# Optimization experiments

Hardware: AMD Instinct MI355X
Metric: run time of the kernel (lower is better)

## Reference

```python
import jax, jax.numpy as jnp
import numpy as np

N_NODES = 50000
N_EDGES = 800000
F_IN = 512
H1 = 64
H2 = 128
N_CLASSES = 10
N_GRAPHS = 64


def _sage_conv(x, src, dst, w_l, b_l, w_r, n_nodes):
    # mean-aggregate neighbor features (messages flow src -> dst), then
    # out = lin_l(mean_neigh) + lin_r(x)   (PyG SAGEConv defaults)
    msg = x[src]                                           # [E, F] gather
    agg = jax.ops.segment_sum(msg, dst, num_segments=n_nodes)
    deg = jax.ops.segment_sum(jnp.ones((src.shape[0], 1), x.dtype), dst,
                              num_segments=n_nodes)
    mean = agg / jnp.maximum(deg, 1.0)                     # 0 for isolated nodes
    return mean @ w_l + b_l + x @ w_r


def setup_inputs() -> dict:
    key = jax.random.key(0)
    ks = jax.random.split(key, 12)
    x = jax.random.normal(ks[0], (N_NODES, F_IN), dtype=jnp.float32)
    edge_index = jax.random.randint(ks[1], (2, N_EDGES), 0, N_NODES, dtype=jnp.int64)
    batch = jnp.sort(jax.random.randint(ks[2], (N_NODES,), 0, N_GRAPHS, dtype=jnp.int64))

    def glorot(k, fan_in, fan_out):
        s = jnp.sqrt(6.0 / (fan_in + fan_out)).astype(jnp.float32)
        return jax.random.uniform(k, (fan_in, fan_out), jnp.float32, -s, s)

    return {
        "x": x, "edge_index": edge_index, "batch": batch,
        "w1_l": glorot(ks[3], F_IN, H1), "b1_l": jnp.zeros((H1,), jnp.float32),
        "w1_r": glorot(ks[4], F_IN, H1),
        "w2_l": glorot(ks[5], H1, H2), "b2_l": jnp.zeros((H2,), jnp.float32),
        "w2_r": glorot(ks[6], H1, H2),
        "w_fc": glorot(ks[7], H2, N_CLASSES),
        "b_fc": jnp.zeros((N_CLASSES,), jnp.float32),
    }


def reference(x, edge_index, batch, w1_l, b1_l, w1_r, w2_l, b2_l, w2_r, w_fc, b_fc):
    src, dst = edge_index[0], edge_index[1]
    n = x.shape[0]
    h = jax.nn.relu(_sage_conv(x, src, dst, w1_l, b1_l, w1_r, n))
    # dropout is identity in eval mode
    h = _sage_conv(h, src, dst, w2_l, b2_l, w2_r, n)        # [N, H2]
    # global mean pool over graphs
    summed = jax.ops.segment_sum(h, batch, num_segments=N_GRAPHS)
    cnt = jax.ops.segment_sum(jnp.ones((n, 1), h.dtype), batch, num_segments=N_GRAPHS)
    pooled = summed / jnp.maximum(cnt, 1.0)                 # [G, H2]
    logits = pooled @ w_fc + b_fc                           # [G, C]
    return jax.nn.log_softmax(logits, axis=1)
```

## Files before the change

### kernel.cpp

```cpp
#include <hip/hip_runtime.h>

#define NN 50000
#define NE 800000
#define FIN 512
#define H1DIM 64
#define H2DIM 128
#define NC 10
#define NG 64
#define NRT 3125
#define SB 196
#define SORT_THREADS (SB * 256)

typedef __attribute__((ext_vector_type(8))) short bf16x8;
typedef __attribute__((ext_vector_type(4))) float f32x4;

__device__ inline short f2bf(float f) {
  unsigned u = __float_as_uint(f);
  unsigned r = u + 0x7fffu + ((u >> 16) & 1u);
  return (short)(r >> 16);
}
__device__ inline float bf2f(short s) {
  return __uint_as_float(((unsigned)(unsigned short)s) << 16);
}

__device__ __forceinline__ void gbar(int* bar, int id) {
  __syncthreads();
  if (threadIdx.x == 0) {
    __threadfence();
    atomicAdd(&bar[id], 1);
    while (atomicAdd(&bar[id], 0) < SB) {}
  }
  __syncthreads();
}

__global__ __launch_bounds__(256) void sort_kernel(
    const int* __restrict__ src, const int* __restrict__ dst,
    int* __restrict__ cnt, int* __restrict__ rowptr, int* __restrict__ cursor,
    int* __restrict__ bsum, int* __restrict__ ssrc, int* __restrict__ bar) {
  const int b = blockIdx.x;
  const int t = threadIdx.x;
  const int idx = b * 256 + t;
  __shared__ int s[256];

  {
    int i = ((b + 98) % SB) * 256 + t;
    if (i < NN) cnt[i] = 0;
  }
  gbar(bar, 0);

  for (int j = idx; j < NE / 4; j += SORT_THREADS) {
    int4 d = *(const int4*)(dst + j * 4);
    atomicAdd(&cnt[d.x], 1);
    atomicAdd(&cnt[d.y], 1);
    atomicAdd(&cnt[d.z], 1);
    atomicAdd(&cnt[d.w], 1);
  }
  gbar(bar, 1);

  int v = (idx < NN) ? atomicAdd(&cnt[idx], 0) : 0;
  s[t] = v;
  __syncthreads();
  for (int off = 1; off < 256; off <<= 1) {
    int u = (t >= off) ? s[t - off] : 0;
    __syncthreads();
    s[t] += u;
    __syncthreads();
  }
  if (idx < NN) rowptr[idx] = s[t] - v;
  if (t == 255) bsum[b] = s[255];
  gbar(bar, 2);

  int bv = (t < SB) ? atomicAdd(&bsum[t], 0) : 0;
  s[t] = bv;
  __syncthreads();
  for (int off = 1; off < 256; off <<= 1) {
    int u = (t >= off) ? s[t - off] : 0;
    __syncthreads();
    s[t] += u;
    __syncthreads();
  }
  int prefix = (b == 0) ? 0 : s[b - 1];
  if (idx < NN) {
    int p = rowptr[idx] + prefix;
    rowptr[idx] = p;
    cursor[idx] = p;
  }
  if (idx == 0) rowptr[NN] = NE;
  gbar(bar, 3);

  for (int j = idx; j < NE / 4; j += SORT_THREADS) {
    int4 sv = *(const int4*)(src + j * 4);
    int4 dv = *(const int4*)(dst + j * 4);
    int p0 = atomicAdd(&cursor[dv.x], 1); ssrc[p0] = sv.x;
    int p1 = atomicAdd(&cursor[dv.y], 1); ssrc[p1] = sv.y;
    int p2 = atomicAdd(&cursor[dv.z], 1); ssrc[p2] = sv.z;
    int p3 = atomicAdd(&cursor[dv.w], 1); ssrc[p3] = sv.w;
  }
}

__global__ __launch_bounds__(256) void wbtf_prep_kernel(
    const float* __restrict__ wl, const float* __restrict__ wr,
    short* __restrict__ wbtf) {
  int w = blockIdx.x * 4 + (threadIdx.x >> 6);
  int lane = threadIdx.x & 63;
  int ni = w >> 4;
  int ks = w & 15;
  int n = ni * 16 + (lane & 15);
  int k = ks * 32 + (lane >> 4) * 8;
  bf16x8 o;
#pragma unroll
  for (int j = 0; j < 8; j++) {
    float v = (n < 64) ? wl[(size_t)(k + j) * 64 + n]
                       : wr[(size_t)(k + j) * 64 + (n - 64)];
    o[j] = f2bf(v);
  }
  *(bf16x8*)(wbtf + ((size_t)w * 64 + lane) * 8) = o;
}

__global__ __launch_bounds__(256) void gemm1_kernel(
    const float* __restrict__ x, const short* __restrict__ wbtf,
    short* __restrict__ xwl, float* __restrict__ xwr) {
  int w = blockIdx.x * 4 + (threadIdx.x >> 6);
  if (w >= NRT) return;
  int lane = threadIdx.x & 63;
  int l15 = lane & 15;
  int q = lane >> 4;
  const float* px = x + (size_t)(w * 16 + l15) * FIN + q * 8;
  const short* pb = wbtf + (size_t)lane * 8;

  const f32x4 z = {0.f, 0.f, 0.f, 0.f};
  f32x4 acc[8];
#pragma unroll
  for (int ni = 0; ni < 8; ni++) acc[ni] = z;

  float4 av0, av1, nv0, nv1;
  bf16x8 B0[8], B1[8];
  av0 = *(const float4*)(px);
  av1 = *(const float4*)(px + 4);
#pragma unroll
  for (int ni = 0; ni < 8; ni++)
    B0[ni] = *(const bf16x8*)(pb + (size_t)ni * 8192);

#pragma unroll
  for (int ks = 0; ks < 16; ks += 2) {
    if (ks + 1 < 16) {
      nv0 = *(const float4*)(px + (ks + 1) * 32);
      nv1 = *(const float4*)(px + (ks + 1) * 32 + 4);
#pragma unroll
      for (int ni = 0; ni < 8; ni++)
        B1[ni] = *(const bf16x8*)(pb + (size_t)ni * 8192 + (ks + 1) * 512);
    }
    {
      bf16x8 af;
      af[0] = f2bf(av0.x); af[1] = f2bf(av0.y);
      af[2] = f2bf(av0.z); af[3] = f2bf(av0.w);
      af[4] = f2bf(av1.x); af[5] = f2bf(av1.y);
      af[6] = f2bf(av1.z); af[7] = f2bf(av1.w);
#pragma unroll
      for (int ni = 0; ni < 8; ni++)
        acc[ni] = __builtin_amdgcn_mfma_f32_16x16x32_bf16(af, B0[ni], acc[ni], 0, 0, 0);
    }
    if (ks + 2 < 16) {
      av0 = *(const float4*)(px + (ks + 2) * 32);
      av1 = *(const float4*)(px + (ks + 2) * 32 + 4);
#pragma unroll
      for (int ni = 0; ni < 8; ni++)
        B0[ni] = *(const bf16x8*)(pb + (size_t)ni * 8192 + (ks + 2) * 512);
    }
    {
      bf16x8 af;
      af[0] = f2bf(nv0.x); af[1] = f2bf(nv0.y);
      af[2] = f2bf(nv0.z); af[3] = f2bf(nv0.w);
      af[4] = f2bf(nv1.x); af[5] = f2bf(nv1.y);
      af[6] = f2bf(nv1.z); af[7] = f2bf(nv1.w);
#pragma unroll
      for (int ni = 0; ni < 8; ni++)
        acc[ni] = __builtin_amdgcn_mfma_f32_16x16x32_bf16(af, B1[ni], acc[ni], 0, 0, 0);
    }
  }

  int row_base = w * 16 + q * 4;
#pragma unroll
  for (int ni = 0; ni < 8; ni++) {
    int col = ni * 16 + l15;
    int c = col & 63;
#pragma unroll
    for (int r = 0; r < 4; r++) {
      int row = row_base + r;
      if (col < 64) xwl[(size_t)row * 64 + c] = f2bf(acc[ni][r]);
      else          xwr[(size_t)row * 64 + c] = acc[ni][r];
    }
  }
}

__global__ __launch_bounds__(256) void agg1_h1_kernel(
    const int* __restrict__ rowptr, const int* __restrict__ ssrc,
    const short* __restrict__ xwl, const float* __restrict__ xwr,
    const float* __restrict__ b1, short* __restrict__ h1) {
  int node = blockIdx.x * 4 + (threadIdx.x >> 6);
  if (node >= NN) return;
  int lane = threadIdx.x & 63;
  int c = lane & 7;
  int r = lane >> 3;
  int lo = rowptr[node], hi = rowptr[node + 1];
  float acc[8];
#pragma unroll
  for (int k = 0; k < 8; k++) acc[k] = 0.f;
  for (int e = lo + r; e < hi; e += 8) {
    int s = ssrc[e];
    bf16x8 v = *(const bf16x8*)(xwl + (size_t)s * 64 + c * 8);
#pragma unroll
    for (int k = 0; k < 8; k++) acc[k] += bf2f(v[k]);
  }
#pragma unroll
  for (int k = 0; k < 8; k++) {
    acc[k] += __shfl_xor(acc[k], 8);
    acc[k] += __shfl_xor(acc[k], 16);
    acc[k] += __shfl_xor(acc[k], 32);
  }
  if (r == 0) {
    float dg = fmaxf((float)(hi - lo), 1.0f);
    const float* xr = xwr + (size_t)node * 64 + c * 8;
    bf16x8 out;
#pragma unroll
    for (int k = 0; k < 8; k++) {
      float v = fmaxf(acc[k] / dg + b1[c * 8 + k] + xr[k], 0.f);
      out[k] = f2bf(v);
    }
    *(bf16x8*)(h1 + (size_t)node * 64 + c * 8) = out;
  }
}

__global__ __launch_bounds__(256) void agg2_kernel(
    const int* __restrict__ rowptr, const int* __restrict__ ssrc,
    const short* __restrict__ h1, float* __restrict__ agg2) {
  int node = blockIdx.x * 4 + (threadIdx.x >> 6);
  if (node >= NN) return;
  int lane = threadIdx.x & 63;
  int c = lane & 7;
  int r = lane >> 3;
  int lo = rowptr[node], hi = rowptr[node + 1];
  float acc[8];
#pragma unroll
  for (int k = 0; k < 8; k++) acc[k] = 0.f;
  for (int e = lo + r; e < hi; e += 8) {
    int s = ssrc[e];
    bf16x8 v = *(const bf16x8*)(h1 + (size_t)s * 64 + c * 8);
#pragma unroll
    for (int k = 0; k < 8; k++) acc[k] += bf2f(v[k]);
  }
#pragma unroll
  for (int k = 0; k < 8; k++) {
    acc[k] += __shfl_xor(acc[k], 8);
    acc[k] += __shfl_xor(acc[k], 16);
    acc[k] += __shfl_xor(acc[k], 32);
  }
  if (r == 0) {
    float* p = agg2 + (size_t)node * 64 + c * 8;
    f32x4 lo4 = {acc[0], acc[1], acc[2], acc[3]};
    f32x4 hi4 = {acc[4], acc[5], acc[6], acc[7]};
    *(f32x4*)(p) = lo4;
    *(f32x4*)(p + 4) = hi4;
  }
}

__global__ __launch_bounds__(256) void pool1_kernel(
    const int* __restrict__ batch, const float* __restrict__ agg2,
    const short* __restrict__ h1, const int* __restrict__ rowptr,
    float* __restrict__ poolA, float* __restrict__ poolB,
    float* __restrict__ poolCnt) {
  int t = threadIdx.x;
  int c = t & 15;
  int s = t >> 4;
  int n0 = blockIdx.x * 256 + s * 16;
  int n1 = n0 + 16;
  if (n1 > NN) n1 = NN;

  f32x4 aA = {0.f, 0.f, 0.f, 0.f};
  f32x4 aB = {0.f, 0.f, 0.f, 0.f};
  int cur_g = -1;
  float run = 0.f;
  for (int n = n0; n < n1; n++) {
    int g = batch[n];
    if (g != cur_g) {
      if (cur_g >= 0) {
        float* pa = poolA + (size_t)cur_g * 64 + c * 4;
        float* pb = poolB + (size_t)cur_g * 64 + c * 4;
#pragma unroll
        for (int k = 0; k < 4; k++) {
          atomicAdd(&pa[k], aA[k]);
          atomicAdd(&pb[k], aB[k]);
        }
        if (c == 0) atomicAdd(&poolCnt[cur_g], run);
      }
      cur_g = g;
      aA = (f32x4){0.f, 0.f, 0.f, 0.f};
      aB = (f32x4){0.f, 0.f, 0.f, 0.f};
      run = 0.f;
    }
    float rd = 1.0f / fmaxf((float)(rowptr[n + 1] - rowptr[n]), 1.0f);
    f32x4 a2 = *(const f32x4*)(agg2 + (size_t)n * 64 + c * 4);
    const short* hp = h1 + (size_t)n * 64 + c * 4;
#pragma unroll
    for (int k = 0; k < 4; k++) {
      aA[k] = fmaf(a2[k], rd, aA[k]);
      aB[k] += bf2f(hp[k]);
    }
    run += 1.f;
  }
  if (cur_g >= 0) {
    float* pa = poolA + (size_t)cur_g * 64 + c * 4;
    float* pb = poolB + (size_t)cur_g * 64 + c * 4;
#pragma unroll
    for (int k = 0; k < 4; k++) {
      atomicAdd(&pa[k], aA[k]);
      atomicAdd(&pb[k], aB[k]);
    }
    if (c == 0) atomicAdd(&poolCnt[cur_g], run);
  }
}

__global__ __launch_bounds__(128) void final_kernel(
    const float* __restrict__ poolA, const float* __restrict__ poolB,
    const float* __restrict__ poolCnt, const float* __restrict__ w2l,
    const float* __restrict__ w2r, const float* __restrict__ b2,
    const float* __restrict__ wfc, const float* __restrict__ bfc,
    float* __restrict__ out) {
  int g = blockIdx.x;
  int j = threadIdx.x;
  __shared__ float sp[H2DIM];
  __shared__ float sl[NC];

  float invc = 1.0f / fmaxf(poolCnt[g], 1.0f);
  float v = b2[j];
  for (int k = 0; k < 64; k++) {
    float a = poolA[g * 64 + k] * invc;
    float b = poolB[g * 64 + k] * invc;
    v = fmaf(a, w2l[k * 128 + j], v);
    v = fmaf(b, w2r[k * 128 + j], v);
  }
  sp[j] = v;
  __syncthreads();
  if (j < NC) {
    float lg = bfc[j];
    for (int k = 0; k < H2DIM; k++) lg = fmaf(sp[k], wfc[k * NC + j], lg);
    sl[j] = lg;
  }
  __syncthreads();
  if (j < NC) {
    float m = -1e30f;
    for (int k = 0; k < NC; k++) m = fmaxf(m, sl[k]);
    float s = 0.f;
    for (int k = 0; k < NC; k++) s += expf(sl[k] - m);
    out[g * NC + j] = sl[j] - m - logf(s);
  }
}

extern "C" void kernel_launch(void* const* d_in, const int* in_sizes, int n_in,
                              void* d_out, int out_size, void* d_ws,
                              size_t ws_size, hipStream_t stream) {
  const float* x   = (const float*)d_in[0];
  const int* edge  = (const int*)d_in[1];
  const int* batch = (const int*)d_in[2];
  const float* w1l = (const float*)d_in[3];
  const float* b1l = (const float*)d_in[4];
  const float* w1r = (const float*)d_in[5];
  const float* w2l = (const float*)d_in[6];
  const float* b2l = (const float*)d_in[7];
  const float* w2r = (const float*)d_in[8];
  const float* wfc = (const float*)d_in[9];
  const float* bfc = (const float*)d_in[10];
  float* out = (float*)d_out;

  const int* src = edge;
  const int* dst = edge + NE;

  const size_t NF = (size_t)NN * 64;
  int*   bar     = (int*)d_ws;
  float* poolA   = (float*)(bar + 8);
  float* poolB   = poolA + (size_t)NG * 64;
  float* poolCnt = poolB + (size_t)NG * 64;
  int*   cnt     = (int*)(poolCnt + NG);
  int*   cursor  = cnt + NN;
  int*   rowptr  = cursor + NN;
  int*   bsum    = rowptr + 50004;
  int*   ssrc    = bsum + 256;
  short* xwl     = (short*)(ssrc + NE);
  short* h1s     = xwl + NF;
  short* wbtf    = h1s + NF;
  float* xwr     = (float*)(wbtf + 65536);
  float* agg2    = xwr + NF;

  hipMemsetAsync(bar, 0, (8 + 2 * NG * 64 + NG) * sizeof(int), stream);

  wbtf_prep_kernel<<<32, 256, 0, stream>>>(w1l, w1r, wbtf);
  sort_kernel<<<SB, 256, 0, stream>>>(src, dst, cnt, rowptr, cursor, bsum, ssrc, bar);
  gemm1_kernel<<<(NRT + 3) / 4, 256, 0, stream>>>(x, wbtf, xwl, xwr);

  agg1_h1_kernel<<<(NN + 3) / 4, 256, 0, stream>>>(rowptr, ssrc, xwl, xwr, b1l, h1s);
  agg2_kernel<<<(NN + 3) / 4, 256, 0, stream>>>(rowptr, ssrc, h1s, agg2);
  pool1_kernel<<<SB, 256, 0, stream>>>(batch, agg2, h1s, rowptr, poolA, poolB, poolCnt);
  final_kernel<<<NG, 128, 0, stream>>>(poolA, poolB, poolCnt, w2l, w2r, b2l, wfc, bfc, out);
}
```

Measured before the change: 414.0 us.

## Split persistent sort kernel with grid barriers into separate launches

Replaces the single persistent CSR-building kernel, which used spin-wait global barriers across 196 blocks, with four separate launches: histogram, block scan, block-sum scan with offset fixup, and scatter. The histogram and scatter kernels now use one thread per four edges over a full grid instead of a grid-stride loop over 196 blocks. The count array is zeroed by the existing memset. This removes the atomic spin-barrier overhead and the under-filled grid, at the cost of three extra kernel launches.

New measurement: 381.0 us. 8.0% less time.

```diff
diff --git a/kernel.cpp b/kernel.cpp
--- a/kernel.cpp
+++ b/kernel.cpp
@@ -8,8 +8,7 @@
 #define NC 10
 #define NG 64
 #define NRT 3125
-#define SB 196
-#define SORT_THREADS (SB * 256)
+#define SCAN_BLOCKS 196
 
 typedef __attribute__((ext_vector_type(8))) short bf16x8;
 typedef __attribute__((ext_vector_type(4))) float f32x4;
@@ -23,41 +22,25 @@
   return __uint_as_float(((unsigned)(unsigned short)s) << 16);
 }
 
-__device__ __forceinline__ void gbar(int* bar, int id) {
-  __syncthreads();
-  if (threadIdx.x == 0) {
-    __threadfence();
-    atomicAdd(&bar[id], 1);
-    while (atomicAdd(&bar[id], 0) < SB) {}
-  }
-  __syncthreads();
-}
-
-__global__ __launch_bounds__(256) void sort_kernel(
-    const int* __restrict__ src, const int* __restrict__ dst,
-    int* __restrict__ cnt, int* __restrict__ rowptr, int* __restrict__ cursor,
-    int* __restrict__ bsum, int* __restrict__ ssrc, int* __restrict__ bar) {
-  const int b = blockIdx.x;
-  const int t = threadIdx.x;
-  const int idx = b * 256 + t;
-  __shared__ int s[256];
-
-  {
-    int i = ((b + 98) % SB) * 256 + t;
-    if (i < NN) cnt[i] = 0;
-  }
-  gbar(bar, 0);
-
-  for (int j = idx; j < NE / 4; j += SORT_THREADS) {
-    int4 d = *(const int4*)(dst + j * 4);
+__global__ __launch_bounds__(256) void hist_kernel(const int* __restrict__ dst,
+                                                   int* __restrict__ cnt) {
+  int i = (blockIdx.x * 256 + threadIdx.x) * 4;
+  if (i < NE) {
+    int4 d = *(const int4*)(dst + i);
     atomicAdd(&cnt[d.x], 1);
     atomicAdd(&cnt[d.y], 1);
     atomicAdd(&cnt[d.z], 1);
     atomicAdd(&cnt[d.w], 1);
   }
-  gbar(bar, 1);
-
-  int v = (idx < NN) ? atomicAdd(&cnt[idx], 0) : 0;
+}
+
+__global__ __launch_bounds__(256) void scan1_kernel(const int* __restrict__ cnt,
+                                                    int* __restrict__ excl,
+                                                    int* __restrict__ bsum) {
+  __shared__ int s[256];
+  int t = threadIdx.x;
+  int i = blockIdx.x * 256 + t;
+  int v = (i < NN) ? cnt[i] : 0;
   s[t] = v;
   __syncthreads();
   for (int off = 1; off < 256; off <<= 1) {
@@ -66,12 +49,18 @@
     s[t] += u;
     __syncthreads();
   }
-  if (idx < NN) rowptr[idx] = s[t] - v;
-  if (t == 255) bsum[b] = s[255];
-  gbar(bar, 2);
-
-  int bv = (t < SB) ? atomicAdd(&bsum[t], 0) : 0;
-  s[t] = bv;
+  if (i < NN) excl[i] = s[t] - v;
+  if (t == 255) bsum[blockIdx.x] = s[255];
+}
+
+__global__ __launch_bounds__(256) void scan23_kernel(const int* __restrict__ bsum,
+                                                     int* __restrict__ rowptr,
+                                                     int* __restrict__ cursor) {
+  __shared__ int s[256];
+  int t = threadIdx.x;
+  int b = blockIdx.x;
+  int v = (t < SCAN_BLOCKS) ? bsum[t] : 0;
+  s[t] = v;
   __syncthreads();
   for (int off = 1; off < 256; off <<= 1) {
     int u = (t >= off) ? s[t - off] : 0;
@@ -80,21 +69,26 @@
     __syncthreads();
   }
   int prefix = (b == 0) ? 0 : s[b - 1];
-  if (idx < NN) {
-    int p = rowptr[idx] + prefix;
-    rowptr[idx] = p;
-    cursor[idx] = p;
-  }
-  if (idx == 0) rowptr[NN] = NE;
-  gbar(bar, 3);
-
-  for (int j = idx; j < NE / 4; j += SORT_THREADS) {
-    int4 sv = *(const int4*)(src + j * 4);
-    int4 dv = *(const int4*)(dst + j * 4);
-    int p0 = atomicAdd(&cursor[dv.x], 1); ssrc[p0] = sv.x;
-    int p1 = atomicAdd(&cursor[dv.y], 1); ssrc[p1] = sv.y;
-    int p2 = atomicAdd(&cursor[dv.z], 1); ssrc[p2] = sv.z;
-    int p3 = atomicAdd(&cursor[dv.w], 1); ssrc[p3] = sv.w;
+  int i = b * 256 + t;
+  if (i < NN) {
+    int p = rowptr[i] + prefix;
+    rowptr[i] = p;
+    cursor[i] = p;
+  }
+  if (i == 0) rowptr[NN] = NE;
+}
+
+__global__ __launch_bounds__(256) void scatter_kernel(
+    const int* __restrict__ src, const int* __restrict__ dst,
+    int* __restrict__ cursor, int* __restrict__ ssrc) {
+  int i = (blockIdx.x * 256 + threadIdx.x) * 4;
+  if (i < NE) {
+    int4 s = *(const int4*)(src + i);
+    int4 d = *(const int4*)(dst + i);
+    int p0 = atomicAdd(&cursor[d.x], 1); ssrc[p0] = s.x;
+    int p1 = atomicAdd(&cursor[d.y], 1); ssrc[p1] = s.y;
+    int p2 = atomicAdd(&cursor[d.z], 1); ssrc[p2] = s.z;
+    int p3 = atomicAdd(&cursor[d.w], 1); ssrc[p3] = s.w;
   }
 }
 
@@ -376,12 +370,11 @@
   const int* dst = edge + NE;
 
   const size_t NF = (size_t)NN * 64;
-  int*   bar     = (int*)d_ws;
-  float* poolA   = (float*)(bar + 8);
+  int*   cnt     = (int*)d_ws;
+  float* poolA   = (float*)(cnt + NN);
   float* poolB   = poolA + (size_t)NG * 64;
   float* poolCnt = poolB + (size_t)NG * 64;
-  int*   cnt     = (int*)(poolCnt + NG);
-  int*   cursor  = cnt + NN;
+  int*   cursor  = (int*)(poolCnt + NG);
   int*   rowptr  = cursor + NN;
   int*   bsum    = rowptr + 50004;
   int*   ssrc    = bsum + 256;
@@ -391,14 +384,18 @@
   float* xwr     = (float*)(wbtf + 65536);
   float* agg2    = xwr + NF;
 
-  hipMemsetAsync(bar, 0, (8 + 2 * NG * 64 + NG) * sizeof(int), stream);
+  hipMemsetAsync(cnt, 0, (NN + 2 * NG * 64 + NG) * sizeof(int), stream);
+
+  hist_kernel<<<(NE / 4 + 255) / 256, 256, 0, stream>>>(dst, cnt);
+  scan1_kernel<<<SCAN_BLOCKS, 256, 0, stream>>>(cnt, rowptr, bsum);
+  scan23_kernel<<<SCAN_BLOCKS, 256, 0, stream>>>(bsum, rowptr, cursor);
+  scatter_kernel<<<(NE / 4 + 255) / 256, 256, 0, stream>>>(src, dst, cursor, ssrc);
 
   wbtf_prep_kernel<<<32, 256, 0, stream>>>(w1l, w1r, wbtf);
-  sort_kernel<<<SB, 256, 0, stream>>>(src, dst, cnt, rowptr, cursor, bsum, ssrc, bar);
   gemm1_kernel<<<(NRT + 3) / 4, 256, 0, stream>>>(x, wbtf, xwl, xwr);
 
   agg1_h1_kernel<<<(NN + 3) / 4, 256, 0, stream>>>(rowptr, ssrc, xwl, xwr, b1l, h1s);
   agg2_kernel<<<(NN + 3) / 4, 256, 0, stream>>>(rowptr, ssrc, h1s, agg2);
-  pool1_kernel<<<SB, 256, 0, stream>>>(batch, agg2, h1s, rowptr, poolA, poolB, poolCnt);
+  pool1_kernel<<<SCAN_BLOCKS, 256, 0, stream>>>(batch, agg2, h1s, rowptr, poolA, poolB, poolCnt);
   final_kernel<<<NG, 128, 0, stream>>>(poolA, poolB, poolCnt, w2l, w2r, b2l, wfc, bfc, out);
 }
```
